# Kernel optimization log

Measured on AMD Instinct MI355X. Metric: run time of the kernel, lower is better.

## Reference

```python
import jax, jax.numpy as jnp
import numpy as np

E = 16        # num_experts
H = 1024      # hidden_size
I = 768       # moe_intermediate_size
TOP_K = 2     # num_experts_per_tok
B, S = 1, 2048


def setup_inputs() -> dict:
    key = jax.random.key(0)
    ks = jax.random.split(key, 5)
    scale = 0.02
    return {
        "hidden_states": jax.random.normal(ks[0], (B, S, H), dtype=jnp.float32),
        "gate_w": jax.random.normal(ks[1], (E, H), dtype=jnp.float32) * scale,
        "gate_proj": jax.random.normal(ks[2], (E, I, H), dtype=jnp.float32) * scale,
        "up_proj": jax.random.normal(ks[3], (E, I, H), dtype=jnp.float32) * scale,
        "down_proj": jax.random.normal(ks[4], (E, H, I), dtype=jnp.float32) * scale,
    }


def reference(hidden_states, gate_w, gate_proj, up_proj, down_proj):
    b, s, h = hidden_states.shape
    x = hidden_states.reshape(-1, h)                        # [T, H]
    T = x.shape[0]

    # Router: logits -> fp32 softmax -> top-k -> renormalize (norm_topk_prob=True)
    router_logits = x @ gate_w.T                            # [T, E]
    probs = jax.nn.softmax(router_logits.astype(jnp.float32), axis=-1)
    top_vals, top_idx = jax.lax.top_k(probs, TOP_K)         # [T, k]
    top_vals = top_vals / jnp.sum(top_vals, axis=-1, keepdims=True)

    # Dense combine-weight matrix [T, E] (zero for unrouted experts)
    rw = jnp.zeros((T, E), dtype=jnp.float32)
    rw = rw.at[jnp.arange(T)[:, None], top_idx].add(top_vals)
    rw = rw.astype(hidden_states.dtype)

    # Expert SwiGLU MLPs (dense-over-experts reference for the grouped GEMM)
    g = jnp.einsum("th,eih->eti", x, gate_proj)             # [E, T, I]
    u = jnp.einsum("th,eih->eti", x, up_proj)               # [E, T, I]
    hmid = jax.nn.silu(g) * u                                # [E, T, I]
    expert_out = jnp.einsum("eti,ehi->eth", hmid, down_proj)  # [E, T, H]

    # Weighted combine
    out = jnp.einsum("eth,te->th", expert_out, rw)          # [T, H]
    return out.reshape(b, s, h)
```

## Files before the change

kernel.cpp:

```cpp
#include <hip/hip_runtime.h>
#include <hip/hip_bf16.h>
#include <cmath>

constexpr int T = 2048;
constexpr int H = 1024;
constexpr int I = 768;
constexpr int E = 16;
constexpr int WMAX = 48;

typedef short short8 __attribute__((ext_vector_type(8)));
typedef float f32x4  __attribute__((ext_vector_type(4)));

__device__ __forceinline__ short f2bf(float f) {
    __hip_bfloat16 h = __float2bfloat16(f);
    return *reinterpret_cast<short*>(&h);
}

__device__ __forceinline__ short8 pack8(float4 a, float4 b) {
    short8 v = {f2bf(a.x), f2bf(a.y), f2bf(a.z), f2bf(a.w),
                f2bf(b.x), f2bf(b.y), f2bf(b.z), f2bf(b.w)};
    return v;
}

__device__ __forceinline__ int sw(int r, int kg) {
    return r * 32 + (((kg + (r >> 1)) & 3) << 3);
}

__global__ __launch_bounds__(256) void cvt_x_kernel(
    const float* __restrict__ x, short* __restrict__ xb)
{
    size_t i = (size_t)blockIdx.x * 256 + threadIdx.x;
    const float4* s4 = (const float4*)x;
    float4 a = s4[2 * i], b = s4[2 * i + 1];
    *(short8*)(xb + i * 8) = pack8(a, b);
}

__global__ __launch_bounds__(256) void router_kernel(
    const float* __restrict__ x,
    const float* __restrict__ gw,
    int* __restrict__ cnt,
    int* __restrict__ entries,
    float* __restrict__ wlist)
{
    const int tid = threadIdx.x;
    const int tl = tid & 15, e = tid >> 4;
    const int t = blockIdx.x * 16 + tl;

    const float4* xr = (const float4*)(x + (size_t)t * H);
    const float4* gr = (const float4*)(gw + (size_t)e * H);
    float s0 = 0.f, s1 = 0.f;
    #pragma unroll 8
    for (int q = 0; q < 256; q += 2) {
        float4 a = xr[q],     b = gr[q];
        float4 c = xr[q + 1], d = gr[q + 1];
        s0 += a.x * b.x + a.y * b.y + a.z * b.z + a.w * b.w;
        s1 += c.x * d.x + c.y * d.y + c.z * d.z + c.w * d.w;
    }

    __shared__ float lg[16][17];
    lg[tl][e] = s0 + s1;
    __syncthreads();

    if (tid < 16) {
        int tk = blockIdx.x * 16 + tid;
        float v1 = -3.0e38f, v2 = -3.0e38f;
        int i1 = 0, i2 = 0;
        #pragma unroll
        for (int k = 0; k < E; ++k) {
            float v = lg[tid][k];
            if (v > v1) { v2 = v1; i2 = i1; v1 = v; i1 = k; }
            else if (v > v2) { v2 = v; i2 = k; }
        }
        float w1 = 1.f / (1.f + expf(v2 - v1));
        float w2 = 1.f - w1;
        int p = atomicAdd(&cnt[i1], 1);
        entries[i1 * T + p] = tk * 2;
        wlist[i1 * T + p] = w1;
        p = atomicAdd(&cnt[i2], 1);
        entries[i2 * T + p] = tk * 2 + 1;
        wlist[i2 * T + p] = w2;
    }
}

__global__ void build_worklist(const int* __restrict__ cnt,
                               int2* __restrict__ items,
                               int* __restrict__ nitems)
{
    if (threadIdx.x == 0) {
        int c = 0;
        for (int e = 0; e < E; ++e) {
            int n = cnt[e];
            for (int t0 = 0; t0 < n; t0 += 128) items[c++] = make_int2(e, t0);
        }
        *nitems = c;
    }
}

__global__ __launch_bounds__(256) void gateup_mfma(
    const short* __restrict__ xb,
    const float* __restrict__ gate_p,
    const float* __restrict__ up_p,
    const int* __restrict__ cnt,
    const int* __restrict__ entries,
    const int* __restrict__ nitems,
    const int2* __restrict__ items,
    short* __restrict__ hmid)
{
    if (blockIdx.x >= *nitems) return;
    const int e  = items[blockIdx.x].x;
    const int t0 = items[blockIdx.x].y;
    const int n  = cnt[e];
    const int i0 = blockIdx.y * 64;

    __shared__ short Xs[128 * 32];
    __shared__ short Gs[64 * 32];
    __shared__ short Us[64 * 32];
    __shared__ int toks[128];

    const int tid = threadIdx.x;
    if (tid < 128) {
        int r = t0 + tid;
        toks[tid] = (r < n) ? entries[e * T + r] : -1;
    }
    __syncthreads();

    const int lane = tid & 63, wave = tid >> 6;
    const int m16 = lane & 15, q = lane >> 4;

    const int sr = tid >> 2, skg = tid & 3;
    const int xt0 = toks[sr], xt1 = toks[64 + sr];
    const short* xsrc0 = xb + (size_t)((xt0 >= 0 ? xt0 : 0) >> 1) * H + skg * 8;
    const short* xsrc1 = xb + (size_t)((xt1 >= 0 ? xt1 : 0) >> 1) * H + skg * 8;
    const float* gsrc = gate_p + (size_t)e * I * H + (size_t)(i0 + sr) * H + skg * 8;
    const float* usrc = up_p   + (size_t)e * I * H + (size_t)(i0 + sr) * H + skg * 8;

    f32x4 accg[8], accu[8];
    #pragma unroll
    for (int a = 0; a < 8; ++a) {
        accg[a] = (f32x4){0.f, 0.f, 0.f, 0.f};
        accu[a] = (f32x4){0.f, 0.f, 0.f, 0.f};
    }

    short8 xc0 = *(const short8*)xsrc0;
    short8 xc1 = *(const short8*)xsrc1;
    float4 gc0 = *(const float4*)gsrc, gc1 = *(const float4*)(gsrc + 4);
    float4 uc0 = *(const float4*)usrc, uc1 = *(const float4*)(usrc + 4);

    for (int k0 = 0; k0 < H; k0 += 32) {
        *(short8*)&Xs[sw(sr, skg)]      = xc0;
        *(short8*)&Xs[sw(64 + sr, skg)] = xc1;
        *(short8*)&Gs[sw(sr, skg)] = pack8(gc0, gc1);
        *(short8*)&Us[sw(sr, skg)] = pack8(uc0, uc1);
        int kn = (k0 + 32 < H) ? k0 + 32 : 0;
        xc0 = *(const short8*)(xsrc0 + kn);
        xc1 = *(const short8*)(xsrc1 + kn);
        gc0 = *(const float4*)(gsrc + kn); gc1 = *(const float4*)(gsrc + kn + 4);
        uc0 = *(const float4*)(usrc + kn); uc1 = *(const float4*)(usrc + kn + 4);
        __syncthreads();

        short8 bg = *(const short8*)&Gs[sw(wave * 16 + m16, q)];
        short8 bu = *(const short8*)&Us[sw(wave * 16 + m16, q)];
        #pragma unroll
        for (int mi = 0; mi < 8; ++mi) {
            short8 af = *(const short8*)&Xs[sw(mi * 16 + m16, q)];
            accg[mi] = __builtin_amdgcn_mfma_f32_16x16x32_bf16(af, bg, accg[mi], 0, 0, 0);
            accu[mi] = __builtin_amdgcn_mfma_f32_16x16x32_bf16(af, bu, accu[mi], 0, 0, 0);
        }
        __syncthreads();
    }

    const int col = i0 + wave * 16 + m16;
    #pragma unroll
    for (int mi = 0; mi < 8; ++mi)
        #pragma unroll
        for (int j = 0; j < 4; ++j) {
            int row = mi * 16 + q * 4 + j;
            int slot = toks[row];
            if (slot < 0) continue;
            float g = accg[mi][j];
            float u = accu[mi][j];
            float hv = g / (1.f + expf(-g)) * u;
            ((unsigned short*)hmid)[(size_t)slot * I + col] = (unsigned short)f2bf(hv);
        }
}

__global__ __launch_bounds__(256) void down_mfma(
    const short* __restrict__ hmid,
    const float* __restrict__ down_p,
    const int* __restrict__ cnt,
    const int* __restrict__ entries,
    const float* __restrict__ wlist,
    const int* __restrict__ nitems,
    const int2* __restrict__ items,
    float* __restrict__ out)
{
    if (blockIdx.x >= *nitems) return;
    const int e  = items[blockIdx.x].x;
    const int t0 = items[blockIdx.x].y;
    const int n  = cnt[e];
    const int h0 = blockIdx.y * 128;

    __shared__ short As[128 * 32];
    __shared__ short Bs[128 * 32];
    __shared__ int toks[128];
    __shared__ float wr[128];

    const int tid = threadIdx.x;
    if (tid < 128) {
        int r = t0 + tid;
        bool v = (r < n);
        toks[tid] = v ? entries[e * T + r] : -1;
        wr[tid]   = v ? wlist[e * T + r] : 0.f;
    }
    __syncthreads();

    const int lane = tid & 63, wave = tid >> 6;
    const int m16 = lane & 15, q = lane >> 4;

    const int sr = tid >> 2, skg = tid & 3;
    const int at0 = toks[sr], at1 = toks[64 + sr];
    const short* asrc0 = hmid + (size_t)(at0 >= 0 ? at0 : 0) * I + skg * 8;
    const short* asrc1 = hmid + (size_t)(at1 >= 0 ? at1 : 0) * I + skg * 8;
    const float* bsrc0 = down_p + (size_t)e * H * I + (size_t)(h0 + sr) * I + skg * 8;
    const float* bsrc1 = down_p + (size_t)e * H * I + (size_t)(h0 + 64 + sr) * I + skg * 8;

    f32x4 acc[8][2];
    #pragma unroll
    for (int a = 0; a < 8; ++a)
        #pragma unroll
        for (int b = 0; b < 2; ++b)
            acc[a][b] = (f32x4){0.f, 0.f, 0.f, 0.f};

    short8 ac0 = *(const short8*)asrc0;
    short8 ac1 = *(const short8*)asrc1;
    float4 bc0 = *(const float4*)bsrc0, bc1 = *(const float4*)(bsrc0 + 4);
    float4 bc2 = *(const float4*)bsrc1, bc3 = *(const float4*)(bsrc1 + 4);

    for (int k0 = 0; k0 < I; k0 += 32) {
        *(short8*)&As[sw(sr, skg)]      = ac0;
        *(short8*)&As[sw(64 + sr, skg)] = ac1;
        *(short8*)&Bs[sw(sr, skg)]      = pack8(bc0, bc1);
        *(short8*)&Bs[sw(64 + sr, skg)] = pack8(bc2, bc3);
        int kn = (k0 + 32 < I) ? k0 + 32 : 0;
        ac0 = *(const short8*)(asrc0 + kn);
        ac1 = *(const short8*)(asrc1 + kn);
        bc0 = *(const float4*)(bsrc0 + kn); bc1 = *(const float4*)(bsrc0 + kn + 4);
        bc2 = *(const float4*)(bsrc1 + kn); bc3 = *(const float4*)(bsrc1 + kn + 4);
        __syncthreads();

        short8 bf0 = *(const short8*)&Bs[sw(wave * 32 + m16, q)];
        short8 bf1 = *(const short8*)&Bs[sw(wave * 32 + 16 + m16, q)];
        #pragma unroll
        for (int mi = 0; mi < 8; ++mi) {
            short8 af = *(const short8*)&As[sw(mi * 16 + m16, q)];
            acc[mi][0] = __builtin_amdgcn_mfma_f32_16x16x32_bf16(af, bf0, acc[mi][0], 0, 0, 0);
            acc[mi][1] = __builtin_amdgcn_mfma_f32_16x16x32_bf16(af, bf1, acc[mi][1], 0, 0, 0);
        }
        __syncthreads();
    }

    #pragma unroll
    for (int mi = 0; mi < 8; ++mi)
        #pragma unroll
        for (int ni = 0; ni < 2; ++ni)
            #pragma unroll
            for (int j = 0; j < 4; ++j) {
                int row = mi * 16 + q * 4 + j;
                int slot = toks[row];
                if (slot < 0) continue;
                int t = slot >> 1;
                float w = wr[row];
                int col = h0 + wave * 32 + ni * 16 + m16;
                atomicAdd(&out[(size_t)t * H + col], w * acc[mi][ni][j]);
            }
}

extern "C" void kernel_launch(void* const* d_in, const int* in_sizes, int n_in,
                              void* d_out, int out_size, void* d_ws, size_t ws_size,
                              hipStream_t stream) {
    const float* x  = (const float*)d_in[0];
    const float* gw = (const float*)d_in[1];
    const float* gp = (const float*)d_in[2];
    const float* up = (const float*)d_in[3];
    const float* dp = (const float*)d_in[4];
    float* out = (float*)d_out;

    char* ws = (char*)d_ws;
    int*   cnt     = (int*)ws;
    int*   nitems  = (int*)(ws + 64);
    int2*  items   = (int2*)(ws + 128);
    int*   entries = (int*)(ws + 2048);
    float* wlist   = (float*)(ws + 2048 + 131072);
    short* xb      = (short*)(ws + 2048 + 262144);
    short* hmid    = xb + (size_t)T * H;

    hipMemsetAsync(ws, 0, 2048, stream);
    hipMemsetAsync(out, 0, (size_t)T * H * sizeof(float), stream);

    cvt_x_kernel<<<T * H / 2048, 256, 0, stream>>>(x, xb);
    router_kernel<<<T / 16, 256, 0, stream>>>(x, gw, cnt, entries, wlist);
    build_worklist<<<1, 64, 0, stream>>>(cnt, items, nitems);
    gateup_mfma<<<dim3(WMAX, I / 64), 256, 0, stream>>>(
        xb, gp, up, cnt, entries, nitems, items, hmid);
    down_mfma<<<dim3(WMAX, H / 128), 256, 0, stream>>>(
        hmid, dp, cnt, entries, wlist, nitems, items, out);
}
```

Before: 309.7 us.

## Fuse x conversion into router, drop worklist kernel, halve GEMM tile widths

The router now writes the bf16 copy of x while it computes the gate logits, so the separate conversion kernel goes away. The single-thread worklist kernel is replaced by each GEMM block scanning the expert counts itself to find its (expert, tile). The gate/up and down GEMM tiles are halved along N to double the grid and raise occupancy. In exchange, each weight tile is reused across fewer blocks and the X/hmid tiles are reloaded more often.

Result: faster. 299.7 us (-3.2%).

```diff
diff --git a/kernel.cpp b/kernel.cpp
--- a/kernel.cpp
+++ b/kernel.cpp
@@ -26,28 +26,35 @@
     return r * 32 + (((kg + (r >> 1)) & 3) << 3);
 }
 
-__global__ __launch_bounds__(256) void cvt_x_kernel(
-    const float* __restrict__ x, short* __restrict__ xb)
-{
-    size_t i = (size_t)blockIdx.x * 256 + threadIdx.x;
-    const float4* s4 = (const float4*)x;
-    float4 a = s4[2 * i], b = s4[2 * i + 1];
-    *(short8*)(xb + i * 8) = pack8(a, b);
-}
-
-__global__ __launch_bounds__(256) void router_kernel(
+__device__ __forceinline__ bool find_item(const int* __restrict__ cnt, int bx,
+                                          int& e_o, int& t0_o, int& n_o) {
+    int c = 0;
+    #pragma unroll
+    for (int e = 0; e < E; ++e) {
+        int n = cnt[e];
+        int m = (n + 127) >> 7;
+        if (bx < c + m) { e_o = e; t0_o = (bx - c) << 7; n_o = n; return true; }
+        c += m;
+    }
+    return false;
+}
+
+__global__ __launch_bounds__(128) void router_kernel(
     const float* __restrict__ x,
     const float* __restrict__ gw,
+    short* __restrict__ xb,
     int* __restrict__ cnt,
     int* __restrict__ entries,
     float* __restrict__ wlist)
 {
     const int tid = threadIdx.x;
-    const int tl = tid & 15, e = tid >> 4;
-    const int t = blockIdx.x * 16 + tl;
+    const int tl = tid & 7, e = tid >> 3;
+    const int t = blockIdx.x * 8 + tl;
 
     const float4* xr = (const float4*)(x + (size_t)t * H);
     const float4* gr = (const float4*)(gw + (size_t)e * H);
+    short* xrow = xb + (size_t)t * H;
+
     float s0 = 0.f, s1 = 0.f;
     #pragma unroll 8
     for (int q = 0; q < 256; q += 2) {
@@ -55,14 +62,16 @@
         float4 c = xr[q + 1], d = gr[q + 1];
         s0 += a.x * b.x + a.y * b.y + a.z * b.z + a.w * b.w;
         s1 += c.x * d.x + c.y * d.y + c.z * d.z + c.w * d.w;
-    }
-
-    __shared__ float lg[16][17];
+        if ((q >> 4) == e)
+            *(short8*)(xrow + q * 4) = pack8(a, c);
+    }
+
+    __shared__ float lg[8][17];
     lg[tl][e] = s0 + s1;
     __syncthreads();
 
-    if (tid < 16) {
-        int tk = blockIdx.x * 16 + tid;
+    if (tid < 8) {
+        int tk = blockIdx.x * 8 + tid;
         float v1 = -3.0e38f, v2 = -3.0e38f;
         int i1 = 0, i2 = 0;
         #pragma unroll
@@ -82,39 +91,21 @@
     }
 }
 
-__global__ void build_worklist(const int* __restrict__ cnt,
-                               int2* __restrict__ items,
-                               int* __restrict__ nitems)
-{
-    if (threadIdx.x == 0) {
-        int c = 0;
-        for (int e = 0; e < E; ++e) {
-            int n = cnt[e];
-            for (int t0 = 0; t0 < n; t0 += 128) items[c++] = make_int2(e, t0);
-        }
-        *nitems = c;
-    }
-}
-
 __global__ __launch_bounds__(256) void gateup_mfma(
     const short* __restrict__ xb,
     const float* __restrict__ gate_p,
     const float* __restrict__ up_p,
     const int* __restrict__ cnt,
     const int* __restrict__ entries,
-    const int* __restrict__ nitems,
-    const int2* __restrict__ items,
     short* __restrict__ hmid)
 {
-    if (blockIdx.x >= *nitems) return;
-    const int e  = items[blockIdx.x].x;
-    const int t0 = items[blockIdx.x].y;
-    const int n  = cnt[e];
-    const int i0 = blockIdx.y * 64;
+    int e, t0, n;
+    if (!find_item(cnt, blockIdx.x, e, t0, n)) return;
+    const int i0 = blockIdx.y * 32;
 
     __shared__ short Xs[128 * 32];
-    __shared__ short Gs[64 * 32];
-    __shared__ short Us[64 * 32];
+    __shared__ short Gs[32 * 32];
+    __shared__ short Us[32 * 32];
     __shared__ int toks[128];
 
     const int tid = threadIdx.x;
@@ -126,55 +117,55 @@
 
     const int lane = tid & 63, wave = tid >> 6;
     const int m16 = lane & 15, q = lane >> 4;
+    const int mh = wave >> 1, ng = wave & 1;
 
     const int sr = tid >> 2, skg = tid & 3;
     const int xt0 = toks[sr], xt1 = toks[64 + sr];
     const short* xsrc0 = xb + (size_t)((xt0 >= 0 ? xt0 : 0) >> 1) * H + skg * 8;
     const short* xsrc1 = xb + (size_t)((xt1 >= 0 ? xt1 : 0) >> 1) * H + skg * 8;
-    const float* gsrc = gate_p + (size_t)e * I * H + (size_t)(i0 + sr) * H + skg * 8;
-    const float* usrc = up_p   + (size_t)e * I * H + (size_t)(i0 + sr) * H + skg * 8;
-
-    f32x4 accg[8], accu[8];
-    #pragma unroll
-    for (int a = 0; a < 8; ++a) {
+    const int wrow = (tid & 127) >> 2;
+    const float* wsrc = (tid >= 128 ? up_p : gate_p)
+        + (size_t)e * I * H + (size_t)(i0 + wrow) * H + skg * 8;
+    short* wdst = (tid >= 128) ? Us : Gs;
+
+    f32x4 accg[4], accu[4];
+    #pragma unroll
+    for (int a = 0; a < 4; ++a) {
         accg[a] = (f32x4){0.f, 0.f, 0.f, 0.f};
         accu[a] = (f32x4){0.f, 0.f, 0.f, 0.f};
     }
 
     short8 xc0 = *(const short8*)xsrc0;
     short8 xc1 = *(const short8*)xsrc1;
-    float4 gc0 = *(const float4*)gsrc, gc1 = *(const float4*)(gsrc + 4);
-    float4 uc0 = *(const float4*)usrc, uc1 = *(const float4*)(usrc + 4);
+    float4 wc0 = *(const float4*)wsrc, wc1 = *(const float4*)(wsrc + 4);
 
     for (int k0 = 0; k0 < H; k0 += 32) {
         *(short8*)&Xs[sw(sr, skg)]      = xc0;
         *(short8*)&Xs[sw(64 + sr, skg)] = xc1;
-        *(short8*)&Gs[sw(sr, skg)] = pack8(gc0, gc1);
-        *(short8*)&Us[sw(sr, skg)] = pack8(uc0, uc1);
+        *(short8*)&wdst[sw(wrow, skg)]  = pack8(wc0, wc1);
         int kn = (k0 + 32 < H) ? k0 + 32 : 0;
         xc0 = *(const short8*)(xsrc0 + kn);
         xc1 = *(const short8*)(xsrc1 + kn);
-        gc0 = *(const float4*)(gsrc + kn); gc1 = *(const float4*)(gsrc + kn + 4);
-        uc0 = *(const float4*)(usrc + kn); uc1 = *(const float4*)(usrc + kn + 4);
-        __syncthreads();
-
-        short8 bg = *(const short8*)&Gs[sw(wave * 16 + m16, q)];
-        short8 bu = *(const short8*)&Us[sw(wave * 16 + m16, q)];
-        #pragma unroll
-        for (int mi = 0; mi < 8; ++mi) {
-            short8 af = *(const short8*)&Xs[sw(mi * 16 + m16, q)];
+        wc0 = *(const float4*)(wsrc + kn); wc1 = *(const float4*)(wsrc + kn + 4);
+        __syncthreads();
+
+        short8 bg = *(const short8*)&Gs[sw(ng * 16 + m16, q)];
+        short8 bu = *(const short8*)&Us[sw(ng * 16 + m16, q)];
+        #pragma unroll
+        for (int mi = 0; mi < 4; ++mi) {
+            short8 af = *(const short8*)&Xs[sw(mh * 64 + mi * 16 + m16, q)];
             accg[mi] = __builtin_amdgcn_mfma_f32_16x16x32_bf16(af, bg, accg[mi], 0, 0, 0);
             accu[mi] = __builtin_amdgcn_mfma_f32_16x16x32_bf16(af, bu, accu[mi], 0, 0, 0);
         }
         __syncthreads();
     }
 
-    const int col = i0 + wave * 16 + m16;
-    #pragma unroll
-    for (int mi = 0; mi < 8; ++mi)
+    const int col = i0 + ng * 16 + m16;
+    #pragma unroll
+    for (int mi = 0; mi < 4; ++mi)
         #pragma unroll
         for (int j = 0; j < 4; ++j) {
-            int row = mi * 16 + q * 4 + j;
+            int row = mh * 64 + mi * 16 + q * 4 + j;
             int slot = toks[row];
             if (slot < 0) continue;
             float g = accg[mi][j];
@@ -190,18 +181,14 @@
     const int* __restrict__ cnt,
     const int* __restrict__ entries,
     const float* __restrict__ wlist,
-    const int* __restrict__ nitems,
-    const int2* __restrict__ items,
     float* __restrict__ out)
 {
-    if (blockIdx.x >= *nitems) return;
-    const int e  = items[blockIdx.x].x;
-    const int t0 = items[blockIdx.x].y;
-    const int n  = cnt[e];
-    const int h0 = blockIdx.y * 128;
+    int e, t0, n;
+    if (!find_item(cnt, blockIdx.x, e, t0, n)) return;
+    const int h0 = blockIdx.y * 64;
 
     __shared__ short As[128 * 32];
-    __shared__ short Bs[128 * 32];
+    __shared__ short Bs[64 * 32];
     __shared__ int toks[128];
     __shared__ float wr[128];
 
@@ -221,58 +208,45 @@
     const int at0 = toks[sr], at1 = toks[64 + sr];
     const short* asrc0 = hmid + (size_t)(at0 >= 0 ? at0 : 0) * I + skg * 8;
     const short* asrc1 = hmid + (size_t)(at1 >= 0 ? at1 : 0) * I + skg * 8;
-    const float* bsrc0 = down_p + (size_t)e * H * I + (size_t)(h0 + sr) * I + skg * 8;
-    const float* bsrc1 = down_p + (size_t)e * H * I + (size_t)(h0 + 64 + sr) * I + skg * 8;
-
-    f32x4 acc[8][2];
-    #pragma unroll
-    for (int a = 0; a < 8; ++a)
-        #pragma unroll
-        for (int b = 0; b < 2; ++b)
-            acc[a][b] = (f32x4){0.f, 0.f, 0.f, 0.f};
+    const float* bsrc = down_p + (size_t)e * H * I + (size_t)(h0 + sr) * I + skg * 8;
+
+    f32x4 acc[8];
+    #pragma unroll
+    for (int a = 0; a < 8; ++a) acc[a] = (f32x4){0.f, 0.f, 0.f, 0.f};
 
     short8 ac0 = *(const short8*)asrc0;
     short8 ac1 = *(const short8*)asrc1;
-    float4 bc0 = *(const float4*)bsrc0, bc1 = *(const float4*)(bsrc0 + 4);
-    float4 bc2 = *(const float4*)bsrc1, bc3 = *(const float4*)(bsrc1 + 4);
+    float4 bc0 = *(const float4*)bsrc, bc1 = *(const float4*)(bsrc + 4);
 
     for (int k0 = 0; k0 < I; k0 += 32) {
         *(short8*)&As[sw(sr, skg)]      = ac0;
         *(short8*)&As[sw(64 + sr, skg)] = ac1;
         *(short8*)&Bs[sw(sr, skg)]      = pack8(bc0, bc1);
-        *(short8*)&Bs[sw(64 + sr, skg)] = pack8(bc2, bc3);
         int kn = (k0 + 32 < I) ? k0 + 32 : 0;
         ac0 = *(const short8*)(asrc0 + kn);
         ac1 = *(const short8*)(asrc1 + kn);
-        bc0 = *(const float4*)(bsrc0 + kn); bc1 = *(const float4*)(bsrc0 + kn + 4);
-        bc2 = *(const float4*)(bsrc1 + kn); bc3 = *(const float4*)(bsrc1 + kn + 4);
-        __syncthreads();
-
-        short8 bf0 = *(const short8*)&Bs[sw(wave * 32 + m16, q)];
-        short8 bf1 = *(const short8*)&Bs[sw(wave * 32 + 16 + m16, q)];
+        bc0 = *(const float4*)(bsrc + kn); bc1 = *(const float4*)(bsrc + kn + 4);
+        __syncthreads();
+
+        short8 bf = *(const short8*)&Bs[sw(wave * 16 + m16, q)];
         #pragma unroll
         for (int mi = 0; mi < 8; ++mi) {
             short8 af = *(const short8*)&As[sw(mi * 16 + m16, q)];
-            acc[mi][0] = __builtin_amdgcn_mfma_f32_16x16x32_bf16(af, bf0, acc[mi][0], 0, 0, 0);
-            acc[mi][1] = __builtin_amdgcn_mfma_f32_16x16x32_bf16(af, bf1, acc[mi][1], 0, 0, 0);
-        }
-        __syncthreads();
-    }
-
+            acc[mi] = __builtin_amdgcn_mfma_f32_16x16x32_bf16(af, bf, acc[mi], 0, 0, 0);
+        }
+        __syncthreads();
+    }
+
+    const int col = h0 + wave * 16 + m16;
     #pragma unroll
     for (int mi = 0; mi < 8; ++mi)
         #pragma unroll
-        for (int ni = 0; ni < 2; ++ni)
-            #pragma unroll
-            for (int j = 0; j < 4; ++j) {
-                int row = mi * 16 + q * 4 + j;
-                int slot = toks[row];
-                if (slot < 0) continue;
-                int t = slot >> 1;
-                float w = wr[row];
-                int col = h0 + wave * 32 + ni * 16 + m16;
-                atomicAdd(&out[(size_t)t * H + col], w * acc[mi][ni][j]);
-            }
+        for (int j = 0; j < 4; ++j) {
+            int row = mi * 16 + q * 4 + j;
+            int slot = toks[row];
+            if (slot < 0) continue;
+            atomicAdd(&out[(size_t)(slot >> 1) * H + col], wr[row] * acc[mi][j]);
+        }
 }
 
 extern "C" void kernel_launch(void* const* d_in, const int* in_sizes, int n_in,
@@ -287,8 +261,6 @@
 
     char* ws = (char*)d_ws;
     int*   cnt     = (int*)ws;
-    int*   nitems  = (int*)(ws + 64);
-    int2*  items   = (int2*)(ws + 128);
     int*   entries = (int*)(ws + 2048);
     float* wlist   = (float*)(ws + 2048 + 131072);
     short* xb      = (short*)(ws + 2048 + 262144);
@@ -297,11 +269,9 @@
     hipMemsetAsync(ws, 0, 2048, stream);
     hipMemsetAsync(out, 0, (size_t)T * H * sizeof(float), stream);
 
-    cvt_x_kernel<<<T * H / 2048, 256, 0, stream>>>(x, xb);
-    router_kernel<<<T / 16, 256, 0, stream>>>(x, gw, cnt, entries, wlist);
-    build_worklist<<<1, 64, 0, stream>>>(cnt, items, nitems);
-    gateup_mfma<<<dim3(WMAX, I / 64), 256, 0, stream>>>(
-        xb, gp, up, cnt, entries, nitems, items, hmid);
-    down_mfma<<<dim3(WMAX, H / 128), 256, 0, stream>>>(
-        hmid, dp, cnt, entries, wlist, nitems, items, out);
-}
+    router_kernel<<<T / 8, 128, 0, stream>>>(x, gw, xb, cnt, entries, wlist);
+    gateup_mfma<<<dim3(WMAX, I / 32), 256, 0, stream>>>(
+        xb, gp, up, cnt, entries, hmid);
+    down_mfma<<<dim3(WMAX, H / 64), 256, 0, stream>>>(
+        hmid, dp, cnt, entries, wlist, out);
+}
```
